# Kernel optimization log

Measured on AMD Instinct MI355X. Metric: run time of the kernel, lower is better.

## Reference

```python
import jax, jax.numpy as jnp
import numpy as np

FS = 5          # filter_size
G = 8           # group_num
C = 64          # n_feats


def conv(x, w, b, pad):
    y = jax.lax.conv_general_dilated(
        x, w, window_strides=(1, 1), padding=[(pad, pad), (pad, pad)],
        dimension_numbers=("NCHW", "OIHW", "NCHW"))
    return y + b[None, :, None, None]


def prelu(x, a):
    return jnp.where(x >= 0, x, a * x)


def extract_patches(x, fs):
    # torch nn.Unfold ordering: channel-major, kernel taps row-major
    p = (fs - 1) // 2
    B, Cc, H, W = x.shape
    xp = jnp.pad(x, ((0, 0), (0, 0), (p, p), (p, p)))
    taps = [xp[:, :, i:i + H, j:j + W] for i in range(fs) for j in range(fs)]
    return jnp.stack(taps, axis=2)  # [B, C, fs*fs, H, W]


def setup_inputs() -> dict:
    key = jax.random.key(0)
    ks = jax.random.split(key, 16)
    s = 0.05
    d = {
        "source": jax.random.normal(ks[0], (2, C, 256, 256), jnp.float32),
        "guidance": jax.random.normal(ks[1], (2, C, 256, 256), jnp.float32),
        # target KG (type='general'): 5x5 s1 + PReLU, 5x5 s1 + PReLU, 1x1 -> fs*fs*g
        "t_w1": jax.random.normal(ks[2], (C, C, 5, 5), jnp.float32) * s,
        "t_b1": jnp.zeros((C,), jnp.float32),
        "t_a1": jnp.float32(0.25),
        "t_w2": jax.random.normal(ks[3], (C, C, 5, 5), jnp.float32) * s,
        "t_b2": jnp.zeros((C,), jnp.float32),
        "t_a2": jnp.float32(0.25),
        "t_w3": jax.random.normal(ks[4], (FS * FS * G, C, 1, 1), jnp.float32) * s,
        "t_b3": jnp.zeros((FS * FS * G,), jnp.float32),
        # guidance KG (type='general')
        "g_w1": jax.random.normal(ks[5], (C, C, 5, 5), jnp.float32) * s,
        "g_b1": jnp.zeros((C,), jnp.float32),
        "g_a1": jnp.float32(0.25),
        "g_w2": jax.random.normal(ks[6], (C, C, 5, 5), jnp.float32) * s,
        "g_b2": jnp.zeros((C,), jnp.float32),
        "g_a2": jnp.float32(0.25),
        "g_w3": jax.random.normal(ks[7], (FS * FS * G, C, 1, 1), jnp.float32) * s,
        "g_b3": jnp.zeros((FS * FS * G,), jnp.float32),
        # jbf_conv: 3x3 + PReLU, 3x3 (no act)
        "j_w1": jax.random.normal(ks[8], (C, C, 3, 3), jnp.float32) * s,
        "j_b1": jnp.zeros((C,), jnp.float32),
        "j_a1": jnp.float32(0.25),
        "j_w2": jax.random.normal(ks[9], (C, C, 3, 3), jnp.float32) * s,
        "j_b2": jnp.zeros((C,), jnp.float32),
    }
    return d


def reference(source, guidance,
              t_w1, t_b1, t_a1, t_w2, t_b2, t_a2, t_w3, t_b3,
              g_w1, g_b1, g_a1, g_w2, g_b2, g_a2, g_w3, g_b3,
              j_w1, j_b1, j_a1, j_w2, j_b2):
    B, Cc, H, W = source.shape
    # target KG
    r = prelu(conv(source, t_w1, t_b1, 2), t_a1)
    r = prelu(conv(r, t_w2, t_b2, 2), t_a2)
    r = conv(r, t_w3, t_b3, 0)                    # [B, fs*fs*g, H, W]
    # guidance KG
    gd = prelu(conv(guidance, g_w1, g_b1, 2), g_a1)
    gd = prelu(conv(gd, g_w2, g_b2, 2), g_a2)
    gd = conv(gd, g_w3, g_b3, 0)                  # [B, fs*fs*g, H, W]
    # per-pixel bilateral kernel
    ker = (r * gd).reshape(B, G, FS * FS, H, W)
    # unfold source and apply kernel: sum over the fs*fs tap dim
    pat = extract_patches(source, FS).reshape(B, G, Cc // G, FS * FS, H, W)
    jbf = jnp.einsum("bgckhw,bgkhw->bgchw", pat, ker).reshape(B, Cc, H, W)
    # output conv pair + residual
    y = prelu(conv(jbf, j_w1, j_b1, 1), j_a1)
    y = conv(y, j_w2, j_b2, 1)
    return y + source
```

## Files before the change

kernel.cpp:

```cpp
#include <hip/hip_runtime.h>

#define CDIM 64
#define HDIM 256
#define WDIM 256
#define HWSZ (HDIM * WDIM)
#define GNUM 8

typedef _Float16 f16;
typedef f16  f16x8  __attribute__((ext_vector_type(8)));
typedef float f32x4 __attribute__((ext_vector_type(4)));

static __device__ __forceinline__ ushort f16bits(float v) {
    f16 h = (f16)v;
    return __builtin_bit_cast(ushort, h);
}

__global__ __launch_bounds__(256) void repack_wf16(const float* __restrict__ w,
                                                   ushort* __restrict__ wt, int TAPS) {
    int idx = blockIdx.x * 256 + threadIdx.x;
    int total = 64 * 64 * TAPS;
    if (idx >= total) return;
    int tap = idx / 4096;
    int rem = idx - tap * 4096;
    int oc = rem >> 6, ic = rem & 63;
    wt[idx] = f16bits(w[(oc * 64 + ic) * TAPS + tap]);
}

__global__ __launch_bounds__(256) void cast_w3(const float* __restrict__ w,
                                               ushort* __restrict__ wt) {
    int idx = blockIdx.x * 256 + threadIdx.x;
    if (idx >= 208 * 64) return;
    int oc = idx >> 6;
    wt[idx] = (oc < 200) ? f16bits(w[idx]) : (ushort)0;
}

template <int KS, bool IN_F32_NCHW, bool PRELU, bool F32OUT>
__global__ __launch_bounds__(256, 2) void conv_mfma(
        const void* __restrict__ inp,
        const ushort* __restrict__ wt,
        const float* __restrict__ bias,
        const float* __restrict__ alpha,
        const float* __restrict__ resid,
        void* __restrict__ outp) {
    constexpr int H  = KS / 2;
    constexpr int TX = 32, TY = 8;
    constexpr int IX = TX + 2 * H, IY = TY + 2 * H;
    constexpr int NP = IX * IY;

    __shared__ __align__(16) ushort sX[NP * 64];

    const int b    = blockIdx.z;
    const int bx   = blockIdx.x * TX;
    const int by   = blockIdx.y * TY;
    const int tid  = threadIdx.x;
    const int lane = tid & 63;
    const int wv   = tid >> 6;
    const int x0w  = (wv & 1) * 16;
    const int y0w  = (wv >> 1) * 4;
    const int lr   = lane & 15;
    const int hi   = lane >> 4;

    if constexpr (IN_F32_NCHW) {
        const float* inf = (const float*)inp + (size_t)b * CDIM * HWSZ;
        for (int i = tid; i < CDIM * NP; i += 256) {
            int ch = i / NP, p = i - ch * NP;
            int iy = p / IX, ix = p - iy * IX;
            int gy = by - H + iy, gx = bx - H + ix;
            float v = 0.f;
            if (gy >= 0 && gy < HDIM && gx >= 0 && gx < WDIM)
                v = inf[ch * HWSZ + gy * WDIM + gx];
            int chunk = (ch >> 3) ^ (ix & 7);
            sX[p * 64 + chunk * 8 + (ch & 7)] = f16bits(v);
        }
    } else {
        const ushort* inh = (const ushort*)inp + (size_t)b * HWSZ * 64;
        for (int i = tid; i < NP * 8; i += 256) {
            int p = i >> 3, chunk = i & 7;
            int iy = p / IX, ix = p - iy * IX;
            int gy = by - H + iy, gx = bx - H + ix;
            uint4 v = make_uint4(0u, 0u, 0u, 0u);
            if (gy >= 0 && gy < HDIM && gx >= 0 && gx < WDIM)
                v = *(const uint4*)(inh + ((size_t)(gy * WDIM + gx)) * 64 + chunk * 8);
            *(uint4*)((char*)sX + p * 128 + ((chunk ^ (ix & 7)) << 4)) = v;
        }
    }
    __syncthreads();

    f32x4 acc[4][4] = {};

    for (int tap = 0; tap < KS * KS; ++tap) {
        const int dy = tap / KS, dx = tap - dy * KS;
        f16x8 bfr[2][4];
#pragma unroll
        for (int ks = 0; ks < 2; ++ks)
#pragma unroll
            for (int nt = 0; nt < 4; ++nt) {
                const ushort* wp = wt + (size_t)tap * 4096 + (nt * 16 + lr) * 64
                                      + ks * 32 + hi * 8;
                bfr[ks][nt] = *(const f16x8*)wp;
            }
#pragma unroll
        for (int ks = 0; ks < 2; ++ks) {
            f16x8 afr[4];
#pragma unroll
            for (int mt = 0; mt < 4; ++mt) {
                int iy = y0w + mt + dy;
                int ix = x0w + dx + lr;
                int chunk = (ks * 4 + hi) ^ (ix & 7);
                afr[mt] = *(const f16x8*)((const char*)sX + (iy * IX + ix) * 128 + (chunk << 4));
            }
#pragma unroll
            for (int mt = 0; mt < 4; ++mt)
#pragma unroll
                for (int nt = 0; nt < 4; ++nt)
                    acc[mt][nt] = __builtin_amdgcn_mfma_f32_16x16x32_f16(
                        afr[mt], bfr[ks][nt], acc[mt][nt], 0, 0, 0);
        }
    }

    const float al = PRELU ? alpha[0] : 0.f;
#pragma unroll
    for (int nt = 0; nt < 4; ++nt) {
        const int oc = nt * 16 + lr;
        const float bs = bias[oc];
#pragma unroll
        for (int mt = 0; mt < 4; ++mt) {
            const int gy = by + y0w + mt;
            const int gxb = bx + x0w + hi * 4;
            if constexpr (!F32OUT) {
                ushort* o = (ushort*)outp + (size_t)b * HWSZ * 64;
#pragma unroll
                for (int r = 0; r < 4; ++r) {
                    float v = acc[mt][nt][r] + bs;
                    if constexpr (PRELU) v = (v >= 0.f) ? v : al * v;
                    o[((size_t)(gy * WDIM + gxb + r)) * 64 + oc] = f16bits(v);
                }
            } else {
                float* o = (float*)outp;
                size_t base = ((size_t)(b * CDIM + oc)) * HWSZ + gy * WDIM + gxb;
                float4 sv = *(const float4*)(resid + base);
                float4 ov;
                ov.x = acc[mt][nt][0] + bs + sv.x;
                ov.y = acc[mt][nt][1] + bs + sv.y;
                ov.z = acc[mt][nt][2] + bs + sv.z;
                ov.w = acc[mt][nt][3] + bs + sv.w;
                *(float4*)(o + base) = ov;
            }
        }
    }
}

__global__ __launch_bounds__(256, 2) void ker_mfma(
        const ushort* __restrict__ r2,
        const ushort* __restrict__ g2,
        const ushort* __restrict__ w3t,
        const float* __restrict__ tb3,
        const ushort* __restrict__ w3g,
        const float* __restrict__ gb3,
        ushort* __restrict__ ker) {
    const int tid  = threadIdx.x;
    const int lane = tid & 63;
    const int wv   = tid >> 6;
    const int lr   = lane & 15;
    const int hi   = lane >> 4;
    const int pixbase = blockIdx.x * 64 + wv * 16;

    f32x4 accr[13] = {}, accg[13] = {};
    const ushort* arb = r2 + (size_t)(pixbase + lr) * 64;
    const ushort* agb = g2 + (size_t)(pixbase + lr) * 64;

#pragma unroll
    for (int ks = 0; ks < 2; ++ks) {
        f16x8 ar = *(const f16x8*)(arb + ks * 32 + hi * 8);
        f16x8 ag = *(const f16x8*)(agb + ks * 32 + hi * 8);
#pragma unroll
        for (int nt = 0; nt < 13; ++nt) {
            f16x8 bt = *(const f16x8*)(w3t + (nt * 16 + lr) * 64 + ks * 32 + hi * 8);
            f16x8 bg = *(const f16x8*)(w3g + (nt * 16 + lr) * 64 + ks * 32 + hi * 8);
            accr[nt] = __builtin_amdgcn_mfma_f32_16x16x32_f16(ar, bt, accr[nt], 0, 0, 0);
            accg[nt] = __builtin_amdgcn_mfma_f32_16x16x32_f16(ag, bg, accg[nt], 0, 0, 0);
        }
    }

#pragma unroll
    for (int nt = 0; nt < 13; ++nt) {
        const int oc = nt * 16 + lr;
        const bool ok = (oc < 200);
        const float bt = ok ? tb3[oc] : 0.f;
        const float bg = ok ? gb3[oc] : 0.f;
#pragma unroll
        for (int r = 0; r < 4; ++r) {
            const int p = pixbase + hi * 4 + r;
            float kv = (accr[nt][r] + bt) * (accg[nt][r] + bg);
            if (ok) ker[(size_t)p * 200 + oc] = f16bits(kv);
        }
    }
}

__global__ __launch_bounds__(256) void jbf_apply(
        const ushort* __restrict__ ker,
        const float* __restrict__ src,
        ushort* __restrict__ out) {
    __shared__ __align__(16) float sSrc[20 * 20 * 8];

    const int g0  = blockIdx.z * 4;
    const int tx0 = blockIdx.x * 16;
    const int ty0 = blockIdx.y * 16;
    const int tid = threadIdx.x;
    const int lx  = tid & 15;
    const int ly  = tid >> 4;
    const int pix = (ty0 + ly) * WDIM + (tx0 + lx);

    for (int gi = 0; gi < 4; ++gi) {
        const int g = g0 + gi;
        __syncthreads();
        for (int i = tid; i < 3200; i += 256) {
            int c   = i / 400;
            int rem = i - c * 400;
            int yy  = rem / 20, xx = rem - yy * 20;
            int gy  = ty0 - 2 + yy, gx = tx0 - 2 + xx;
            float v = 0.f;
            if (gy >= 0 && gy < HDIM && gx >= 0 && gx < WDIM)
                v = src[(size_t)(g * 8 + c) * HWSZ + gy * WDIM + gx];
            sSrc[(yy * 20 + xx) * 8 + c] = v;
        }
        __syncthreads();

        float kt[25];
        const ushort* kp = ker + (size_t)pix * 200 + g * 25;
#pragma unroll
        for (int t = 0; t < 25; ++t)
            kt[t] = (float)(*(const f16*)(kp + t));

        float a8[8] = {};
#pragma unroll
        for (int t = 0; t < 25; ++t) {
            const int dy = t / 5, dx = t - dy * 5;
            const float* sp = &sSrc[((ly + dy) * 20 + (lx + dx)) * 8];
            f32x4 v0 = *(const f32x4*)sp;
            f32x4 v1 = *(const f32x4*)(sp + 4);
#pragma unroll
            for (int c = 0; c < 4; ++c) {
                a8[c]     = fmaf(kt[t], v0[c], a8[c]);
                a8[c + 4] = fmaf(kt[t], v1[c], a8[c + 4]);
            }
        }

        f16x8 h;
#pragma unroll
        for (int c = 0; c < 8; ++c) h[c] = (f16)a8[c];
        *(uint4*)(out + (size_t)pix * 64 + g * 8) = __builtin_bit_cast(uint4, h);
    }
}

extern "C" void kernel_launch(void* const* d_in, const int* in_sizes, int n_in,
                              void* d_out, int out_size, void* d_ws, size_t ws_size,
                              hipStream_t stream) {
    const float* source   = (const float*)d_in[0];
    const float* guidance = (const float*)d_in[1];
    const float* t_w1 = (const float*)d_in[2];
    const float* t_b1 = (const float*)d_in[3];
    const float* t_a1 = (const float*)d_in[4];
    const float* t_w2 = (const float*)d_in[5];
    const float* t_b2 = (const float*)d_in[6];
    const float* t_a2 = (const float*)d_in[7];
    const float* t_w3 = (const float*)d_in[8];
    const float* t_b3 = (const float*)d_in[9];
    const float* g_w1 = (const float*)d_in[10];
    const float* g_b1 = (const float*)d_in[11];
    const float* g_a1 = (const float*)d_in[12];
    const float* g_w2 = (const float*)d_in[13];
    const float* g_b2 = (const float*)d_in[14];
    const float* g_a2 = (const float*)d_in[15];
    const float* g_w3 = (const float*)d_in[16];
    const float* g_b3 = (const float*)d_in[17];
    const float* j_w1 = (const float*)d_in[18];
    const float* j_b1 = (const float*)d_in[19];
    const float* j_a1 = (const float*)d_in[20];
    const float* j_w2 = (const float*)d_in[21];
    const float* j_b2 = (const float*)d_in[22];

    const size_t planeH  = (size_t)2 * HWSZ * 64;
    const size_t halfH   = (size_t)HWSZ * 64;
    ushort* bufA  = (ushort*)d_ws;
    ushort* bufB  = bufA + planeH;
    ushort* kerB  = bufB + planeH;
    ushort* wt_t1 = kerB + (size_t)HWSZ * 200;
    ushort* wt_t2 = wt_t1 + 102400;
    ushort* wt_g1 = wt_t2 + 102400;
    ushort* wt_g2 = wt_g1 + 102400;
    ushort* wt_j1 = wt_g2 + 102400;
    ushort* wt_j2 = wt_j1 + 36864;
    ushort* w3t   = wt_j2 + 36864;
    ushort* w3g   = w3t + 13312;
    ushort* bufC  = (ushort*)d_out;

    repack_wf16<<<(64 * 64 * 25 + 255) / 256, 256, 0, stream>>>(t_w1, wt_t1, 25);
    repack_wf16<<<(64 * 64 * 25 + 255) / 256, 256, 0, stream>>>(t_w2, wt_t2, 25);
    repack_wf16<<<(64 * 64 * 25 + 255) / 256, 256, 0, stream>>>(g_w1, wt_g1, 25);
    repack_wf16<<<(64 * 64 * 25 + 255) / 256, 256, 0, stream>>>(g_w2, wt_g2, 25);
    repack_wf16<<<(64 * 64 * 9 + 255) / 256, 256, 0, stream>>>(j_w1, wt_j1, 9);
    repack_wf16<<<(64 * 64 * 9 + 255) / 256, 256, 0, stream>>>(j_w2, wt_j2, 9);
    cast_w3<<<(208 * 64 + 255) / 256, 256, 0, stream>>>(t_w3, w3t);
    cast_w3<<<(208 * 64 + 255) / 256, 256, 0, stream>>>(g_w3, w3g);

    dim3 cgrid(WDIM / 32, HDIM / 8, 2);
    dim3 blk(256);

    conv_mfma<5, true,  true,  false><<<cgrid, blk, 0, stream>>>(source,   wt_t1, t_b1, t_a1, nullptr, bufA);
    conv_mfma<5, false, true,  false><<<cgrid, blk, 0, stream>>>(bufA,     wt_t2, t_b2, t_a2, nullptr, bufB);
    conv_mfma<5, true,  true,  false><<<cgrid, blk, 0, stream>>>(guidance, wt_g1, g_b1, g_a1, nullptr, bufA);
    conv_mfma<5, false, true,  false><<<cgrid, blk, 0, stream>>>(bufA,     wt_g2, g_b2, g_a2, nullptr, bufC);

    dim3 agrid(HDIM / 16, WDIM / 16, 2);
    for (int b = 0; b < 2; ++b) {
        ker_mfma<<<dim3(HWSZ / 64), blk, 0, stream>>>(
            bufB + b * halfH, bufC + b * halfH, w3t, t_b3, w3g, g_b3, kerB);
        jbf_apply<<<agrid, blk, 0, stream>>>(
            kerB, source + (size_t)b * CDIM * HWSZ, bufA + b * halfH);
    }

    conv_mfma<3, false, true,  false><<<cgrid, blk, 0, stream>>>(bufA, wt_j1, j_b1, j_a1, nullptr, bufB);
    conv_mfma<3, false, false, true ><<<cgrid, blk, 0, stream>>>(bufB, wt_j2, j_b2, nullptr, source, d_out);
}
```

Measured before the change: 649.5 us.

## Stage per-tap conv weights into LDS with double-buffered async loads

Conv weights for each tap are now copied cooperatively into a double-buffered shared-memory area with global_load_lds, prefetching the next tap while the current one is computed. Previously every wave loaded the full per-tap weight block from global memory into registers. The repack kernel now writes weights in an XOR-swizzled layout so the LDS B-fragment reads avoid bank conflicts. The cost is a block-wide barrier every tap, plus 16 KB more LDS per block, which could limit occupancy.

```diff
diff --git a/kernel.cpp b/kernel.cpp
--- a/kernel.cpp
+++ b/kernel.cpp
@@ -23,7 +23,9 @@
     int tap = idx / 4096;
     int rem = idx - tap * 4096;
     int oc = rem >> 6, ic = rem & 63;
-    wt[idx] = f16bits(w[(oc * 64 + ic) * TAPS + tap]);
+    int chunk = ic >> 3, j = ic & 7;
+    int dst = tap * 4096 + oc * 64 + ((chunk ^ (oc & 7)) << 3) + j;
+    wt[dst] = f16bits(w[(oc * 64 + ic) * TAPS + tap]);
 }
 
 __global__ __launch_bounds__(256) void cast_w3(const float* __restrict__ w,
@@ -42,12 +44,14 @@
         const float* __restrict__ alpha,
         const float* __restrict__ resid,
         void* __restrict__ outp) {
-    constexpr int H  = KS / 2;
+    constexpr int H    = KS / 2;
+    constexpr int TAPS = KS * KS;
     constexpr int TX = 32, TY = 8;
     constexpr int IX = TX + 2 * H, IY = TY + 2 * H;
     constexpr int NP = IX * IY;
 
     __shared__ __align__(16) ushort sX[NP * 64];
+    __shared__ __align__(16) ushort sW[2][4096];
 
     const int b    = blockIdx.z;
     const int bx   = blockIdx.x * TX;
@@ -60,6 +64,18 @@
     const int lr   = lane & 15;
     const int hi   = lane >> 4;
 
+    auto stageW = [&](int tap, int bufSel) {
+        const ushort* gs = wt + (size_t)tap * 4096 + wv * 1024 + lane * 8;
+        ushort* ls = &sW[bufSel][wv * 1024];
+        __builtin_amdgcn_global_load_lds(
+            (const __attribute__((address_space(1))) void*)gs,
+            (__attribute__((address_space(3))) void*)ls, 16, 0, 0);
+        __builtin_amdgcn_global_load_lds(
+            (const __attribute__((address_space(1))) void*)(gs + 512),
+            (__attribute__((address_space(3))) void*)(ls + 512), 16, 0, 0);
+    };
+
+    stageW(0, 0);
     if constexpr (IN_F32_NCHW) {
         const float* inf = (const float*)inp + (size_t)b * CDIM * HWSZ;
         for (int i = tid; i < CDIM * NP; i += 256) {
@@ -88,20 +104,13 @@
 
     f32x4 acc[4][4] = {};
 
-    for (int tap = 0; tap < KS * KS; ++tap) {
+    for (int tap = 0; tap < TAPS; ++tap) {
+        const int cur = tap & 1;
+        if (tap + 1 < TAPS) stageW(tap + 1, cur ^ 1);
         const int dy = tap / KS, dx = tap - dy * KS;
-        f16x8 bfr[2][4];
-#pragma unroll
-        for (int ks = 0; ks < 2; ++ks)
-#pragma unroll
-            for (int nt = 0; nt < 4; ++nt) {
-                const ushort* wp = wt + (size_t)tap * 4096 + (nt * 16 + lr) * 64
-                                      + ks * 32 + hi * 8;
-                bfr[ks][nt] = *(const f16x8*)wp;
-            }
 #pragma unroll
         for (int ks = 0; ks < 2; ++ks) {
-            f16x8 afr[4];
+            f16x8 afr[4], bfr[4];
 #pragma unroll
             for (int mt = 0; mt < 4; ++mt) {
                 int iy = y0w + mt + dy;
@@ -110,12 +119,19 @@
                 afr[mt] = *(const f16x8*)((const char*)sX + (iy * IX + ix) * 128 + (chunk << 4));
             }
 #pragma unroll
+            for (int nt = 0; nt < 4; ++nt) {
+                int csw = (ks * 4 + hi) ^ (lr & 7);
+                bfr[nt] = *(const f16x8*)((const char*)&sW[cur][0]
+                             + (nt * 16 + lr) * 128 + (csw << 4));
+            }
+#pragma unroll
             for (int mt = 0; mt < 4; ++mt)
 #pragma unroll
                 for (int nt = 0; nt < 4; ++nt)
                     acc[mt][nt] = __builtin_amdgcn_mfma_f32_16x16x32_f16(
-                        afr[mt], bfr[ks][nt], acc[mt][nt], 0, 0, 0);
-        }
+                        afr[mt], bfr[nt], acc[mt][nt], 0, 0, 0);
+        }
+        __syncthreads();
     }
 
     const float al = PRELU ? alpha[0] : 0.f;
```

Measured after the change: 533.7 us. -17.8%, faster.

## Use zero-padded NHWC fp16 buffers and cache-streamed convs without LDS staging

Applied to the files above, without the earlier changes.

Adds a one-time pass that converts source and guidance into zero-padded (260x260) NHWC fp16 planes, and makes every intermediate buffer padded too. The convolution kernels can then load MFMA A-fragments straight from global memory with no bounds checks, shared-memory tile or __syncthreads. The old path did slow strided fp32 NCHW gathers into LDS. Tiles shrink to 32x4 pixels per block and the launch bound asks for 3 blocks per CU, relying on L1/L2 to serve the overlapping halo reads. The risk is higher cache traffic per tap, since each wave reloads A fragments from global memory for every tap.

```diff
diff --git a/kernel.cpp b/kernel.cpp
--- a/kernel.cpp
+++ b/kernel.cpp
@@ -4,7 +4,9 @@
 #define HDIM 256
 #define WDIM 256
 #define HWSZ (HDIM * WDIM)
-#define GNUM 8
+#define PAD 2
+#define PW 260
+#define PPLANE ((size_t)PW * PW * 64)
 
 typedef _Float16 f16;
 typedef f16  f16x8  __attribute__((ext_vector_type(8)));
@@ -18,8 +20,7 @@
 __global__ __launch_bounds__(256) void repack_wf16(const float* __restrict__ w,
                                                    ushort* __restrict__ wt, int TAPS) {
     int idx = blockIdx.x * 256 + threadIdx.x;
-    int total = 64 * 64 * TAPS;
-    if (idx >= total) return;
+    if (idx >= 64 * 64 * TAPS) return;
     int tap = idx / 4096;
     int rem = idx - tap * 4096;
     int oc = rem >> 6, ic = rem & 63;
@@ -34,88 +35,84 @@
     wt[idx] = (oc < 200) ? f16bits(w[idx]) : (ushort)0;
 }
 
-template <int KS, bool IN_F32_NCHW, bool PRELU, bool F32OUT>
-__global__ __launch_bounds__(256, 2) void conv_mfma(
-        const void* __restrict__ inp,
+__global__ __launch_bounds__(256) void padc(const float* __restrict__ in,
+                                            ushort* __restrict__ out) {
+    int id = blockIdx.x * 256 + threadIdx.x;
+    if (id >= PW * PW) return;
+    const int b = blockIdx.z;
+    int py = id / PW, px = id - py * PW;
+    ushort* o = out + (size_t)b * PPLANE + (size_t)id * 64;
+    int y = py - PAD, x = px - PAD;
+    if (y >= 0 && y < HDIM && x >= 0 && x < WDIM) {
+        const float* ib = in + (size_t)b * CDIM * HWSZ + y * WDIM + x;
+#pragma unroll
+        for (int c8 = 0; c8 < 8; ++c8) {
+            f16x8 h;
+#pragma unroll
+            for (int j = 0; j < 8; ++j) h[j] = (f16)ib[(size_t)(c8 * 8 + j) * HWSZ];
+            *(uint4*)(o + c8 * 8) = __builtin_bit_cast(uint4, h);
+        }
+    } else {
+        uint4 z = make_uint4(0u, 0u, 0u, 0u);
+#pragma unroll
+        for (int c8 = 0; c8 < 8; ++c8) *(uint4*)(o + c8 * 8) = z;
+    }
+}
+
+__global__ __launch_bounds__(256) void zfill(uint4* __restrict__ p, size_t n4) {
+    size_t i = (size_t)blockIdx.x * 256 + threadIdx.x;
+    const size_t stride = (size_t)gridDim.x * 256;
+    uint4 z = make_uint4(0u, 0u, 0u, 0u);
+    for (; i < n4; i += stride) p[i] = z;
+}
+
+template <int KS, bool PRELU, bool F32OUT>
+__global__ __launch_bounds__(256, 3) void conv_stream(
+        const ushort* __restrict__ in,
         const ushort* __restrict__ wt,
         const float* __restrict__ bias,
         const float* __restrict__ alpha,
         const float* __restrict__ resid,
         void* __restrict__ outp) {
-    constexpr int H  = KS / 2;
-    constexpr int TX = 32, TY = 8;
-    constexpr int IX = TX + 2 * H, IY = TY + 2 * H;
-    constexpr int NP = IX * IY;
-
-    __shared__ __align__(16) ushort sX[NP * 64];
-
-    const int b    = blockIdx.z;
-    const int bx   = blockIdx.x * TX;
-    const int by   = blockIdx.y * TY;
-    const int tid  = threadIdx.x;
+    constexpr int H = KS / 2;
+    const int b   = blockIdx.z;
+    const int x0  = blockIdx.x * 32;
+    const int y0  = blockIdx.y * 4;
+    const int tid = threadIdx.x;
     const int lane = tid & 63;
-    const int wv   = tid >> 6;
-    const int x0w  = (wv & 1) * 16;
-    const int y0w  = (wv >> 1) * 4;
-    const int lr   = lane & 15;
-    const int hi   = lane >> 4;
-
-    if constexpr (IN_F32_NCHW) {
-        const float* inf = (const float*)inp + (size_t)b * CDIM * HWSZ;
-        for (int i = tid; i < CDIM * NP; i += 256) {
-            int ch = i / NP, p = i - ch * NP;
-            int iy = p / IX, ix = p - iy * IX;
-            int gy = by - H + iy, gx = bx - H + ix;
-            float v = 0.f;
-            if (gy >= 0 && gy < HDIM && gx >= 0 && gx < WDIM)
-                v = inf[ch * HWSZ + gy * WDIM + gx];
-            int chunk = (ch >> 3) ^ (ix & 7);
-            sX[p * 64 + chunk * 8 + (ch & 7)] = f16bits(v);
-        }
-    } else {
-        const ushort* inh = (const ushort*)inp + (size_t)b * HWSZ * 64;
-        for (int i = tid; i < NP * 8; i += 256) {
-            int p = i >> 3, chunk = i & 7;
-            int iy = p / IX, ix = p - iy * IX;
-            int gy = by - H + iy, gx = bx - H + ix;
-            uint4 v = make_uint4(0u, 0u, 0u, 0u);
-            if (gy >= 0 && gy < HDIM && gx >= 0 && gx < WDIM)
-                v = *(const uint4*)(inh + ((size_t)(gy * WDIM + gx)) * 64 + chunk * 8);
-            *(uint4*)((char*)sX + p * 128 + ((chunk ^ (ix & 7)) << 4)) = v;
-        }
-    }
-    __syncthreads();
-
-    f32x4 acc[4][4] = {};
-
+    const int wv  = tid >> 6;
+    const int lr  = lane & 15;
+    const int hi  = lane >> 4;
+
+    const ushort* inb = in + (size_t)b * PPLANE
+        + ((size_t)(y0 + wv + PAD - H) * PW + (x0 + PAD - H)) * 64;
+
+    f32x4 acc[2][4] = {};
+
+#pragma unroll
     for (int tap = 0; tap < KS * KS; ++tap) {
         const int dy = tap / KS, dx = tap - dy * KS;
-        f16x8 bfr[2][4];
+        const ushort* ar = inb + (dy * PW + dx) * 64;
+        const ushort* wr = wt + tap * 4096;
+        f16x8 a[2][2], bf[4][2];
+#pragma unroll
+        for (int mf = 0; mf < 2; ++mf)
+#pragma unroll
+            for (int ks = 0; ks < 2; ++ks)
+                a[mf][ks] = *(const f16x8*)(ar + (mf * 16 + lr) * 64 + ks * 32 + hi * 8);
+#pragma unroll
+        for (int nt = 0; nt < 4; ++nt)
+#pragma unroll
+            for (int ks = 0; ks < 2; ++ks)
+                bf[nt][ks] = *(const f16x8*)(wr + (nt * 16 + lr) * 64 + ks * 32 + hi * 8);
 #pragma unroll
         for (int ks = 0; ks < 2; ++ks)
 #pragma unroll
-            for (int nt = 0; nt < 4; ++nt) {
-                const ushort* wp = wt + (size_t)tap * 4096 + (nt * 16 + lr) * 64
-                                      + ks * 32 + hi * 8;
-                bfr[ks][nt] = *(const f16x8*)wp;
-            }
-#pragma unroll
-        for (int ks = 0; ks < 2; ++ks) {
-            f16x8 afr[4];
-#pragma unroll
-            for (int mt = 0; mt < 4; ++mt) {
-                int iy = y0w + mt + dy;
-                int ix = x0w + dx + lr;
-                int chunk = (ks * 4 + hi) ^ (ix & 7);
-                afr[mt] = *(const f16x8*)((const char*)sX + (iy * IX + ix) * 128 + (chunk << 4));
-            }
-#pragma unroll
-            for (int mt = 0; mt < 4; ++mt)
+            for (int mf = 0; mf < 2; ++mf)
 #pragma unroll
                 for (int nt = 0; nt < 4; ++nt)
-                    acc[mt][nt] = __builtin_amdgcn_mfma_f32_16x16x32_f16(
-                        afr[mt], bfr[ks][nt], acc[mt][nt], 0, 0, 0);
-        }
+                    acc[mf][nt] = __builtin_amdgcn_mfma_f32_16x16x32_f16(
+                        a[mf][ks], bf[nt][ks], acc[mf][nt], 0, 0, 0);
     }
 
     const float al = PRELU ? alpha[0] : 0.f;
@@ -124,26 +121,26 @@
         const int oc = nt * 16 + lr;
         const float bs = bias[oc];
 #pragma unroll
-        for (int mt = 0; mt < 4; ++mt) {
-            const int gy = by + y0w + mt;
-            const int gxb = bx + x0w + hi * 4;
+        for (int mf = 0; mf < 2; ++mf) {
             if constexpr (!F32OUT) {
-                ushort* o = (ushort*)outp + (size_t)b * HWSZ * 64;
+                ushort* ob = (ushort*)outp + (size_t)b * PPLANE
+                    + ((size_t)(y0 + wv + PAD) * PW + (x0 + mf * 16 + hi * 4 + PAD)) * 64 + oc;
 #pragma unroll
                 for (int r = 0; r < 4; ++r) {
-                    float v = acc[mt][nt][r] + bs;
+                    float v = acc[mf][nt][r] + bs;
                     if constexpr (PRELU) v = (v >= 0.f) ? v : al * v;
-                    o[((size_t)(gy * WDIM + gxb + r)) * 64 + oc] = f16bits(v);
+                    ob[(size_t)r * 64] = f16bits(v);
                 }
             } else {
                 float* o = (float*)outp;
-                size_t base = ((size_t)(b * CDIM + oc)) * HWSZ + gy * WDIM + gxb;
+                size_t base = ((size_t)(b * CDIM + oc)) * HWSZ
+                            + (size_t)(y0 + wv) * WDIM + x0 + mf * 16 + hi * 4;
                 float4 sv = *(const float4*)(resid + base);
                 float4 ov;
-                ov.x = acc[mt][nt][0] + bs + sv.x;
-                ov.y = acc[mt][nt][1] + bs + sv.y;
-                ov.z = acc[mt][nt][2] + bs + sv.z;
-                ov.w = acc[mt][nt][3] + bs + sv.w;
+                ov.x = acc[mf][nt][0] + bs + sv.x;
+                ov.y = acc[mf][nt][1] + bs + sv.y;
+                ov.z = acc[mf][nt][2] + bs + sv.z;
+                ov.w = acc[mf][nt][3] + bs + sv.w;
                 *(float4*)(o + base) = ov;
             }
         }
@@ -164,11 +161,13 @@
     const int lr   = lane & 15;
     const int hi   = lane >> 4;
     const int pixbase = blockIdx.x * 64 + wv * 16;
+    const int y = pixbase >> 8, x0p = pixbase & 255;
+
+    const size_t rowoff = ((size_t)(y + PAD) * PW + (x0p + PAD)) * 64;
+    const ushort* arb = r2 + rowoff + (size_t)lr * 64;
+    const ushort* agb = g2 + rowoff + (size_t)lr * 64;
 
     f32x4 accr[13] = {}, accg[13] = {};
-    const ushort* arb = r2 + (size_t)(pixbase + lr) * 64;
-    const ushort* agb = g2 + (size_t)(pixbase + lr) * 64;
-
 #pragma unroll
     for (int ks = 0; ks < 2; ++ks) {
         f16x8 ar = *(const f16x8*)(arb + ks * 32 + hi * 8);
@@ -181,7 +180,6 @@
             accg[nt] = __builtin_amdgcn_mfma_f32_16x16x32_f16(ag, bg, accg[nt], 0, 0, 0);
         }
     }
-
 #pragma unroll
     for (int nt = 0; nt < 13; ++nt) {
         const int oc = nt * 16 + lr;
@@ -210,6 +208,7 @@
     const int lx  = tid & 15;
     const int ly  = tid >> 4;
     const int pix = (ty0 + ly) * WDIM + (tx0 + lx);
+    ushort* op = out + ((size_t)(ty0 + ly + PAD) * PW + (tx0 + lx + PAD)) * 64;
 
     for (int gi = 0; gi < 4; ++gi) {
         const int g = g0 + gi;
@@ -245,11 +244,10 @@
                 a8[c + 4] = fmaf(kt[t], v1[c], a8[c + 4]);
             }
         }
-
         f16x8 h;
 #pragma unroll
         for (int c = 0; c < 8; ++c) h[c] = (f16)a8[c];
-        *(uint4*)(out + (size_t)pix * 64 + g * 8) = __builtin_bit_cast(uint4, h);
+        *(uint4*)(op + g * 8) = __builtin_bit_cast(uint4, h);
     }
 }
 
@@ -280,12 +278,10 @@
     const float* j_w2 = (const float*)d_in[21];
     const float* j_b2 = (const float*)d_in[22];
 
-    const size_t planeH  = (size_t)2 * HWSZ * 64;
-    const size_t halfH   = (size_t)HWSZ * 64;
-    ushort* bufA  = (ushort*)d_ws;
-    ushort* bufB  = bufA + planeH;
-    ushort* kerB  = bufB + planeH;
-    ushort* wt_t1 = kerB + (size_t)HWSZ * 200;
+    ushort* P1    = (ushort*)d_ws;
+    ushort* P2    = P1 + 2 * PPLANE;
+    ushort* P3    = P2 + 2 * PPLANE;
+    ushort* wt_t1 = P3 + 2 * PPLANE;
     ushort* wt_t2 = wt_t1 + 102400;
     ushort* wt_g1 = wt_t2 + 102400;
     ushort* wt_g2 = wt_g1 + 102400;
@@ -293,7 +289,7 @@
     ushort* wt_j2 = wt_j1 + 36864;
     ushort* w3t   = wt_j2 + 36864;
     ushort* w3g   = w3t + 13312;
-    ushort* bufC  = (ushort*)d_out;
+    ushort* kerB  = (ushort*)d_out;
 
     repack_wf16<<<(64 * 64 * 25 + 255) / 256, 256, 0, stream>>>(t_w1, wt_t1, 25);
     repack_wf16<<<(64 * 64 * 25 + 255) / 256, 256, 0, stream>>>(t_w2, wt_t2, 25);
@@ -304,22 +300,26 @@
     cast_w3<<<(208 * 64 + 255) / 256, 256, 0, stream>>>(t_w3, w3t);
     cast_w3<<<(208 * 64 + 255) / 256, 256, 0, stream>>>(g_w3, w3g);
 
-    dim3 cgrid(WDIM / 32, HDIM / 8, 2);
     dim3 blk(256);
-
-    conv_mfma<5, true,  true,  false><<<cgrid, blk, 0, stream>>>(source,   wt_t1, t_b1, t_a1, nullptr, bufA);
-    conv_mfma<5, false, true,  false><<<cgrid, blk, 0, stream>>>(bufA,     wt_t2, t_b2, t_a2, nullptr, bufB);
-    conv_mfma<5, true,  true,  false><<<cgrid, blk, 0, stream>>>(guidance, wt_g1, g_b1, g_a1, nullptr, bufA);
-    conv_mfma<5, false, true,  false><<<cgrid, blk, 0, stream>>>(bufA,     wt_g2, g_b2, g_a2, nullptr, bufC);
+    dim3 pgrid((PW * PW + 255) / 256, 1, 2);
+    padc<<<pgrid, blk, 0, stream>>>(source, P1);
+    padc<<<pgrid, blk, 0, stream>>>(guidance, P2);
+    zfill<<<dim3(2048), blk, 0, stream>>>((uint4*)P3, (2 * PPLANE) / 8);
+
+    dim3 cgrid(WDIM / 32, HDIM / 4, 2);
+    conv_stream<5, true,  false><<<cgrid, blk, 0, stream>>>(P1, wt_t1, t_b1, t_a1, nullptr, P3);
+    conv_stream<5, true,  false><<<cgrid, blk, 0, stream>>>(P3, wt_t2, t_b2, t_a2, nullptr, P1);
+    conv_stream<5, true,  false><<<cgrid, blk, 0, stream>>>(P2, wt_g1, g_b1, g_a1, nullptr, P3);
+    conv_stream<5, true,  false><<<cgrid, blk, 0, stream>>>(P3, wt_g2, g_b2, g_a2, nullptr, P2);
 
     dim3 agrid(HDIM / 16, WDIM / 16, 2);
     for (int b = 0; b < 2; ++b) {
         ker_mfma<<<dim3(HWSZ / 64), blk, 0, stream>>>(
-            bufB + b * halfH, bufC + b * halfH, w3t, t_b3, w3g, g_b3, kerB);
+            P1 + b * PPLANE, P2 + b * PPLANE, w3t, t_b3, w3g, g_b3, kerB);
         jbf_apply<<<agrid, blk, 0, stream>>>(
-            kerB, source + (size_t)b * CDIM * HWSZ, bufA + b * halfH);
-    }
-
-    conv_mfma<3, false, true,  false><<<cgrid, blk, 0, stream>>>(bufA, wt_j1, j_b1, j_a1, nullptr, bufB);
-    conv_mfma<3, false, false, true ><<<cgrid, blk, 0, stream>>>(bufB, wt_j2, j_b2, nullptr, source, d_out);
-}
+            kerB, source + (size_t)b * CDIM * HWSZ, P3 + b * PPLANE);
+    }
+
+    conv_stream<3, true,  false><<<cgrid, blk, 0, stream>>>(P3, wt_j1, j_b1, j_a1, nullptr, P1);
+    conv_stream<3, false, true ><<<cgrid, blk, 0, stream>>>(P1, wt_j2, j_b2, nullptr, source, d_out);
+}
```

New measurement: 974.8 us. 50.1% more time.
